# Optimization experiments

Measured on AMD Instinct MI355X. Metric: run time of the kernel, lower is better.

## Reference

```python
import jax, jax.numpy as jnp
import numpy as np
from jax import lax

B, C, H, W = 16, 256, 96, 96
G, K, RED = 4, 3, 4


def setup_inputs() -> dict:
    key = jax.random.key(0)
    ks = jax.random.split(key, 8)
    return {
        "x": jax.random.normal(ks[0], (B, C, H, W), jnp.float32),
        "w_k": jax.random.normal(ks[1], (G, C, K, K), jnp.float32) * 0.02,
        "b_k": jax.random.normal(ks[2], (G, C), jnp.float32) * 0.02,
        "w1": jax.random.normal(ks[3], (C // RED, C), jnp.float32) * 0.05,
        "b1": jax.random.normal(ks[4], (C // RED,), jnp.float32) * 0.02,
        "bn_g": jnp.ones((C // RED,), jnp.float32),
        "bn_b": jnp.zeros((C // RED,), jnp.float32),
        "bn_m": jnp.zeros((C // RED,), jnp.float32),
        "bn_v": jnp.ones((C // RED,), jnp.float32),
        "w2": jax.random.normal(ks[5], (C * G, C // RED), jnp.float32) * 0.05,
        "b2": jax.random.normal(ks[6], (C * G,), jnp.float32) * 0.02,
    }


def reference(x, w_k, b_k, w1, b1, bn_g, bn_b, bn_m, bn_v, w2, b2):
    eps = 1e-5

    def proj(t):  # t: (B, C, h, w) -> (B, C*G, h, w)
        h = jnp.einsum('oc,bchw->bohw', w1, t) + b1[None, :, None, None]
        h = (h - bn_m[None, :, None, None]) * (bn_g / jnp.sqrt(bn_v + eps))[None, :, None, None] + bn_b[None, :, None, None]
        h = jax.nn.gelu(h, approximate=False)
        return jnp.einsum('oc,bchw->bohw', w2, h) + b2[None, :, None, None]

    # AdaptiveAvgPool2d((K, K)) with H, W divisible by K -> uniform block mean
    pooled = x.reshape(B, C, K, H // K, K, W // K).mean(axis=(3, 5))  # (B, C, K, K)
    scale = proj(pooled).reshape(B, G, C, K, K)
    scale = jax.nn.softmax(scale, axis=1)
    weight = jnp.einsum('bgckl,gckl->bckl', scale, w_k)  # (B, C, K, K) dynamic depthwise kernels

    # dynamic bias from global average pooling
    s2 = proj(x.mean(axis=(2, 3), keepdims=True)).reshape(B, G, C)
    s2 = jax.nn.softmax(s2, axis=1)
    bias = jnp.einsum('bgc,gc->bc', s2, b_k)  # (B, C)

    pad = K // 2

    def conv_one(xb, wb):  # xb (C,H,W), wb (C,K,K): depthwise conv, SAME padding
        return lax.conv_general_dilated(
            xb[None], wb[:, None], window_strides=(1, 1),
            padding=[(pad, pad), (pad, pad)], feature_group_count=C)[0]

    out = jax.vmap(conv_one)(x, weight) + bias[:, :, None, None]
    return out
```

## Files before the change

kernel.cpp:

```cpp
#include <hip/hip_runtime.h>
#include <math.h>

#define BB 16
#define CC 256
#define HH 96
#define WW 96
#define TS 104

typedef float floatx4 __attribute__((ext_vector_type(4)));

__global__ __launch_bounds__(256) void pool_kernel(const float* __restrict__ x,
                                                   float* __restrict__ pooled) {
    const int bc = blockIdx.x;
    const float4* p4 = (const float4*)(x + (size_t)bc * (HH * WW));
    const int tid  = threadIdx.x;
    const int lane = tid & 63;
    const int wv   = tid >> 6;
    const int r_in = tid >> 3;
    const int c4   = tid & 7;
    __shared__ float red[9][4];

    float s[9];
    #pragma unroll
    for (int bi = 0; bi < 3; ++bi)
        #pragma unroll
        for (int bj = 0; bj < 3; ++bj) {
            float4 v = p4[(bi * 32 + r_in) * 24 + bj * 8 + c4];
            s[bi * 3 + bj] = v.x + v.y + v.z + v.w;
        }

    #pragma unroll
    for (int k = 0; k < 9; ++k) {
        float t = s[k];
        #pragma unroll
        for (int off = 32; off; off >>= 1) t += __shfl_down(t, off, 64);
        if (lane == 0) red[k][wv] = t;
    }
    __syncthreads();
    if (tid < 9)
        pooled[bc * 9 + tid] =
            (red[tid][0] + red[tid][1] + red[tid][2] + red[tid][3]) * (1.0f / 1024.0f);
}

__global__ __launch_bounds__(256) void proj_kernel(
    const float* __restrict__ pooled,
    const float* __restrict__ w1, const float* __restrict__ b1,
    const float* __restrict__ bn_g, const float* __restrict__ bn_b,
    const float* __restrict__ bn_m, const float* __restrict__ bn_v,
    const float* __restrict__ w2, const float* __restrict__ b2,
    const float* __restrict__ w_k, const float* __restrict__ b_k,
    float* __restrict__ weight, float* __restrict__ bias) {
    const int b = blockIdx.x / 10;
    const int p = blockIdx.x % 10;
    const int tid = threadIdx.x;

    __shared__ __align__(16) float t[CC];
    __shared__ __align__(16) float hbuf[64];
    __shared__ float hpart[256];

    if (p < 9) {
        t[tid] = pooled[(b * CC + tid) * 9 + p];
    } else {
        float s = 0.f;
        #pragma unroll
        for (int q = 0; q < 9; ++q) s += pooled[(b * CC + tid) * 9 + q];
        t[tid] = s * (1.0f / 9.0f);
    }
    __syncthreads();

    const int o = tid & 63, part = tid >> 6;
    {
        const float4* w1r = (const float4*)(w1 + o * CC + part * 64);
        const float4* tp  = (const float4*)(t + part * 64);
        float acc = 0.f;
        #pragma unroll
        for (int k = 0; k < 16; ++k) {
            float4 a = w1r[k], v = tp[k];
            acc += a.x * v.x + a.y * v.y + a.z * v.z + a.w * v.w;
        }
        hpart[tid] = acc;
    }
    __syncthreads();
    if (tid < 64) {
        float hsum = hpart[tid] + hpart[tid + 64] + hpart[tid + 128] +
                     hpart[tid + 192] + b1[tid];
        float hn = (hsum - bn_m[tid]) * (bn_g[tid] * rsqrtf(bn_v[tid] + 1e-5f)) + bn_b[tid];
        hbuf[tid] = 0.5f * hn * (1.0f + erff(hn * 0.70710678118654752f));
    }
    __syncthreads();

    float vals[4];
    #pragma unroll
    for (int q = 0; q < 4; ++q) {
        const int j = q * 256 + tid;
        const float4* w2r = (const float4*)(w2 + j * 64);
        const float4* hb  = (const float4*)hbuf;
        float a = b2[j];
        #pragma unroll
        for (int k = 0; k < 16; ++k) {
            float4 wv = w2r[k], hv = hb[k];
            a += wv.x * hv.x + wv.y * hv.y + wv.z * hv.z + wv.w * hv.w;
        }
        vals[q] = a;
    }
    float m = fmaxf(fmaxf(vals[0], vals[1]), fmaxf(vals[2], vals[3]));
    float e[4], sum = 0.f;
    #pragma unroll
    for (int q = 0; q < 4; ++q) { e[q] = expf(vals[q] - m); sum += e[q]; }
    const float rinv = 1.0f / sum;

    if (p < 9) {
        float ws = 0.f;
        #pragma unroll
        for (int q = 0; q < 4; ++q)
            ws += (e[q] * rinv) * w_k[(q * CC + tid) * 9 + p];
        weight[(b * CC + tid) * 9 + p] = ws;
    } else {
        float bs = 0.f;
        #pragma unroll
        for (int q = 0; q < 4; ++q)
            bs += (e[q] * rinv) * b_k[q * CC + tid];
        bias[b * CC + tid] = bs;
    }
}

__global__ __launch_bounds__(256) void dwconv_kernel(
    const float* __restrict__ x, const float* __restrict__ weight,
    const float* __restrict__ bias, float* __restrict__ out) {
    const int bc   = blockIdx.x >> 1;
    const int half = blockIdx.x & 1;
    const int r0   = half * 48;
    const float* plane = x + (size_t)bc * (HH * WW);
    float* oplane = out + (size_t)bc * (HH * WW);
    __shared__ __align__(16) float tile[50 * TS];
    const int tid = threadIdx.x;

    if (tid < 50) {
        tile[tid * TS + 3]   = 0.f;
        tile[tid * TS + 100] = 0.f;
    }
    if (tid < 98)
        tile[(half ? 49 * TS : 0) + 3 + tid] = 0.f;

    float wgt[9];
    #pragma unroll
    for (int k = 0; k < 9; ++k) wgt[k] = weight[bc * 9 + k];
    const float bs = bias[bc];

    {
        const int gstart = half ? 47 : 0;
        const int trow0  = half ? 0 : 1;
        const float4* p4 = (const float4*)plane + gstart * 24;
        float4* t4 = (float4*)tile + trow0 * (TS / 4);
        #pragma unroll
        for (int i = 0; i < 5; ++i) {
            const int idx4 = tid + 256 * i;
            if (idx4 < 1176) {
                const int r  = idx4 / 24;
                const int c4 = idx4 - r * 24;
                t4[r * (TS / 4) + 1 + c4] = p4[r * 24 + c4];
            }
        }
    }
    __syncthreads();

    #pragma unroll
    for (int j = 0; j < 2; ++j) {
        const int pidx = tid + 256 * j;
        if (pidx < 288) {
            const int pr = pidx / 24;
            const int pc = pidx - pr * 24;
            const int h0 = pr * 4;
            const int cb = 4 + pc * 4;

            float4 m[6]; float L[6], R[6];
            #pragma unroll
            for (int r = 0; r < 6; ++r) {
                const int a = (h0 + r) * TS + cb;
                m[r] = *(const float4*)(tile + a);
                L[r] = tile[a - 1];
                R[r] = tile[a + 4];
            }
            #pragma unroll
            for (int orow = 0; orow < 4; ++orow) {
                floatx4 acc = {bs, bs, bs, bs};
                #pragma unroll
                for (int r = 0; r < 3; ++r) {
                    const int rr = orow + r;
                    const float wl = wgt[r * 3 + 0], wc = wgt[r * 3 + 1],
                                wr = wgt[r * 3 + 2];
                    acc.x += wl * L[rr]   + wc * m[rr].x + wr * m[rr].y;
                    acc.y += wl * m[rr].x + wc * m[rr].y + wr * m[rr].z;
                    acc.z += wl * m[rr].y + wc * m[rr].z + wr * m[rr].w;
                    acc.w += wl * m[rr].z + wc * m[rr].w + wr * R[rr];
                }
                __builtin_nontemporal_store(
                    acc, (floatx4*)(oplane + (r0 + h0 + orow) * 96 + (cb - 4)));
            }
        }
    }
}

extern "C" void kernel_launch(void* const* d_in, const int* in_sizes, int n_in,
                              void* d_out, int out_size, void* d_ws, size_t ws_size,
                              hipStream_t stream) {
    const float* x    = (const float*)d_in[0];
    const float* w_k  = (const float*)d_in[1];
    const float* b_k  = (const float*)d_in[2];
    const float* w1   = (const float*)d_in[3];
    const float* b1   = (const float*)d_in[4];
    const float* bn_g = (const float*)d_in[5];
    const float* bn_b = (const float*)d_in[6];
    const float* bn_m = (const float*)d_in[7];
    const float* bn_v = (const float*)d_in[8];
    const float* w2   = (const float*)d_in[9];
    const float* b2   = (const float*)d_in[10];
    float* out = (float*)d_out;

    float* pooled = (float*)d_ws;
    float* weight = pooled + BB * CC * 9;
    float* bias   = weight + BB * CC * 9;

    pool_kernel<<<BB * CC, 256, 0, stream>>>(x, pooled);
    proj_kernel<<<BB * 10, 256, 0, stream>>>(pooled, w1, b1, bn_g, bn_b, bn_m,
                                             bn_v, w2, b2, w_k, b_k, weight, bias);
    dwconv_kernel<<<BB * CC * 2, 256, 0, stream>>>(x, weight, bias, out);
}
```

Baseline: 315.3 us.

## Fuse pool, projection and depthwise conv into one cooperative persistent kernel

Replaces the three separate launches with a single cooperative kernel that runs the pooling, projection/softmax and depthwise conv stages in grid-stride loops separated by grid-wide syncs. The aim is to remove inter-kernel launch gaps and tail effects. In exchange, the grid is limited to resident blocks, most blocks idle during the small projection stage, and the combined shared memory footprint may reduce occupancy. The three-kernel path is kept as a fallback if the cooperative launch fails.

```diff
diff --git a/kernel.cpp b/kernel.cpp
--- a/kernel.cpp
+++ b/kernel.cpp
@@ -1,5 +1,8 @@
 #include <hip/hip_runtime.h>
+#include <hip/hip_cooperative_groups.h>
 #include <math.h>
+
+namespace cg = cooperative_groups;
 
 #define BB 16
 #define CC 256
@@ -8,6 +11,205 @@
 #define TS 104
 
 typedef float floatx4 __attribute__((ext_vector_type(4)));
+
+__global__ __launch_bounds__(256) void fused_kernel(
+    const float* __restrict__ x,
+    const float* __restrict__ w_k, const float* __restrict__ b_k,
+    const float* __restrict__ w1, const float* __restrict__ b1,
+    const float* __restrict__ bn_g, const float* __restrict__ bn_b,
+    const float* __restrict__ bn_m, const float* __restrict__ bn_v,
+    const float* __restrict__ w2, const float* __restrict__ b2,
+    float* __restrict__ pooled, float* __restrict__ weight,
+    float* __restrict__ bias, float* __restrict__ out) {
+
+    __shared__ __align__(16) float tile[50 * TS];
+    __shared__ __align__(16) float t[CC];
+    __shared__ __align__(16) float hbuf[64];
+    __shared__ float hpart[256];
+    __shared__ float red[9][4];
+
+    const int tid  = threadIdx.x;
+    const int lane = tid & 63;
+    const int wv   = tid >> 6;
+    cg::grid_group grid = cg::this_grid();
+
+    {
+        const int r_in = tid >> 3;
+        const int c4   = tid & 7;
+        for (int bc = blockIdx.x; bc < BB * CC; bc += gridDim.x) {
+            const float4* p4 = (const float4*)(x + (size_t)bc * (HH * WW));
+            float s[9];
+            #pragma unroll
+            for (int bi = 0; bi < 3; ++bi)
+                #pragma unroll
+                for (int bj = 0; bj < 3; ++bj) {
+                    float4 v = p4[(bi * 32 + r_in) * 24 + bj * 8 + c4];
+                    s[bi * 3 + bj] = v.x + v.y + v.z + v.w;
+                }
+            #pragma unroll
+            for (int k = 0; k < 9; ++k) {
+                float tv = s[k];
+                #pragma unroll
+                for (int off = 32; off; off >>= 1) tv += __shfl_down(tv, off, 64);
+                if (lane == 0) red[k][wv] = tv;
+            }
+            __syncthreads();
+            if (tid < 9)
+                pooled[bc * 9 + tid] =
+                    (red[tid][0] + red[tid][1] + red[tid][2] + red[tid][3]) * (1.0f / 1024.0f);
+            __syncthreads();
+        }
+    }
+    __threadfence();
+    grid.sync();
+
+    for (int u = blockIdx.x; u < BB * 10; u += gridDim.x) {
+        const int b = u / 10;
+        const int p = u % 10;
+
+        if (p < 9) {
+            t[tid] = pooled[(b * CC + tid) * 9 + p];
+        } else {
+            float s = 0.f;
+            #pragma unroll
+            for (int q = 0; q < 9; ++q) s += pooled[(b * CC + tid) * 9 + q];
+            t[tid] = s * (1.0f / 9.0f);
+        }
+        __syncthreads();
+
+        const int o = tid & 63, part = tid >> 6;
+        {
+            const float4* w1r = (const float4*)(w1 + o * CC + part * 64);
+            const float4* tp  = (const float4*)(t + part * 64);
+            float acc = 0.f;
+            #pragma unroll
+            for (int k = 0; k < 16; ++k) {
+                float4 a = w1r[k], v = tp[k];
+                acc += a.x * v.x + a.y * v.y + a.z * v.z + a.w * v.w;
+            }
+            hpart[tid] = acc;
+        }
+        __syncthreads();
+        if (tid < 64) {
+            float hsum = hpart[tid] + hpart[tid + 64] + hpart[tid + 128] +
+                         hpart[tid + 192] + b1[tid];
+            float hn = (hsum - bn_m[tid]) * (bn_g[tid] * rsqrtf(bn_v[tid] + 1e-5f)) + bn_b[tid];
+            hbuf[tid] = 0.5f * hn * (1.0f + erff(hn * 0.70710678118654752f));
+        }
+        __syncthreads();
+
+        float vals[4];
+        #pragma unroll
+        for (int q = 0; q < 4; ++q) {
+            const int j = q * 256 + tid;
+            const float4* w2r = (const float4*)(w2 + j * 64);
+            const float4* hb  = (const float4*)hbuf;
+            float a = b2[j];
+            #pragma unroll
+            for (int k = 0; k < 16; ++k) {
+                float4 wvv = w2r[k], hv = hb[k];
+                a += wvv.x * hv.x + wvv.y * hv.y + wvv.z * hv.z + wvv.w * hv.w;
+            }
+            vals[q] = a;
+        }
+        float m = fmaxf(fmaxf(vals[0], vals[1]), fmaxf(vals[2], vals[3]));
+        float e[4], sum = 0.f;
+        #pragma unroll
+        for (int q = 0; q < 4; ++q) { e[q] = expf(vals[q] - m); sum += e[q]; }
+        const float rinv = 1.0f / sum;
+
+        if (p < 9) {
+            float ws = 0.f;
+            #pragma unroll
+            for (int q = 0; q < 4; ++q)
+                ws += (e[q] * rinv) * w_k[(q * CC + tid) * 9 + p];
+            weight[(b * CC + tid) * 9 + p] = ws;
+        } else {
+            float bs = 0.f;
+            #pragma unroll
+            for (int q = 0; q < 4; ++q)
+                bs += (e[q] * rinv) * b_k[q * CC + tid];
+            bias[b * CC + tid] = bs;
+        }
+        __syncthreads();
+    }
+    __threadfence();
+    grid.sync();
+
+    for (int hp = blockIdx.x; hp < BB * CC * 2; hp += gridDim.x) {
+        __syncthreads();
+        const int bc   = hp >> 1;
+        const int half = hp & 1;
+        const int r0   = half * 48;
+        const float* plane = x + (size_t)bc * (HH * WW);
+        float* oplane = out + (size_t)bc * (HH * WW);
+
+        if (tid < 50) {
+            tile[tid * TS + 3]   = 0.f;
+            tile[tid * TS + 100] = 0.f;
+        }
+        if (tid < 98)
+            tile[(half ? 49 * TS : 0) + 3 + tid] = 0.f;
+
+        float wgt[9];
+        #pragma unroll
+        for (int k = 0; k < 9; ++k) wgt[k] = weight[bc * 9 + k];
+        const float bs = bias[bc];
+
+        {
+            const int gstart = half ? 47 : 0;
+            const int trow0  = half ? 0 : 1;
+            const float4* p4 = (const float4*)plane + gstart * 24;
+            float4* t4 = (float4*)tile + trow0 * (TS / 4);
+            #pragma unroll
+            for (int i = 0; i < 5; ++i) {
+                const int idx4 = tid + 256 * i;
+                if (idx4 < 1176) {
+                    const int r  = idx4 / 24;
+                    const int c4 = idx4 - r * 24;
+                    t4[r * (TS / 4) + 1 + c4] = p4[r * 24 + c4];
+                }
+            }
+        }
+        __syncthreads();
+
+        #pragma unroll
+        for (int j = 0; j < 2; ++j) {
+            const int pidx = tid + 256 * j;
+            if (pidx < 288) {
+                const int pr = pidx / 24;
+                const int pc = pidx - pr * 24;
+                const int h0 = pr * 4;
+                const int cb = 4 + pc * 4;
+
+                float4 m[6]; float L[6], R[6];
+                #pragma unroll
+                for (int r = 0; r < 6; ++r) {
+                    const int a = (h0 + r) * TS + cb;
+                    m[r] = *(const float4*)(tile + a);
+                    L[r] = tile[a - 1];
+                    R[r] = tile[a + 4];
+                }
+                #pragma unroll
+                for (int orow = 0; orow < 4; ++orow) {
+                    floatx4 acc = {bs, bs, bs, bs};
+                    #pragma unroll
+                    for (int r = 0; r < 3; ++r) {
+                        const int rr = orow + r;
+                        const float wl = wgt[r * 3 + 0], wc = wgt[r * 3 + 1],
+                                    wr = wgt[r * 3 + 2];
+                        acc.x += wl * L[rr]   + wc * m[rr].x + wr * m[rr].y;
+                        acc.y += wl * m[rr].x + wc * m[rr].y + wr * m[rr].z;
+                        acc.z += wl * m[rr].y + wc * m[rr].z + wr * m[rr].w;
+                        acc.w += wl * m[rr].z + wc * m[rr].w + wr * R[rr];
+                    }
+                    __builtin_nontemporal_store(
+                        acc, (floatx4*)(oplane + (r0 + h0 + orow) * 96 + (cb - 4)));
+                }
+            }
+        }
+    }
+}
 
 __global__ __launch_bounds__(256) void pool_kernel(const float* __restrict__ x,
                                                    float* __restrict__ pooled) {
@@ -28,13 +230,12 @@
             float4 v = p4[(bi * 32 + r_in) * 24 + bj * 8 + c4];
             s[bi * 3 + bj] = v.x + v.y + v.z + v.w;
         }
-
     #pragma unroll
     for (int k = 0; k < 9; ++k) {
-        float t = s[k];
-        #pragma unroll
-        for (int off = 32; off; off >>= 1) t += __shfl_down(t, off, 64);
-        if (lane == 0) red[k][wv] = t;
+        float tv = s[k];
+        #pragma unroll
+        for (int off = 32; off; off >>= 1) tv += __shfl_down(tv, off, 64);
+        if (lane == 0) red[k][wv] = tv;
     }
     __syncthreads();
     if (tid < 9)
@@ -67,7 +268,6 @@
         t[tid] = s * (1.0f / 9.0f);
     }
     __syncthreads();
-
     const int o = tid & 63, part = tid >> 6;
     {
         const float4* w1r = (const float4*)(w1 + o * CC + part * 64);
@@ -88,7 +288,6 @@
         hbuf[tid] = 0.5f * hn * (1.0f + erff(hn * 0.70710678118654752f));
     }
     __syncthreads();
-
     float vals[4];
     #pragma unroll
     for (int q = 0; q < 4; ++q) {
@@ -98,8 +297,8 @@
         float a = b2[j];
         #pragma unroll
         for (int k = 0; k < 16; ++k) {
-            float4 wv = w2r[k], hv = hb[k];
-            a += wv.x * hv.x + wv.y * hv.y + wv.z * hv.z + wv.w * hv.w;
+            float4 wvv = w2r[k], hv = hb[k];
+            a += wvv.x * hv.x + wvv.y * hv.y + wvv.z * hv.z + wvv.w * hv.w;
         }
         vals[q] = a;
     }
@@ -108,7 +307,6 @@
     #pragma unroll
     for (int q = 0; q < 4; ++q) { e[q] = expf(vals[q] - m); sum += e[q]; }
     const float rinv = 1.0f / sum;
-
     if (p < 9) {
         float ws = 0.f;
         #pragma unroll
@@ -172,7 +370,6 @@
             const int pc = pidx - pr * 24;
             const int h0 = pr * 4;
             const int cb = 4 + pc * 4;
-
             float4 m[6]; float L[6], R[6];
             #pragma unroll
             for (int r = 0; r < 6; ++r) {
@@ -221,8 +418,32 @@
     float* weight = pooled + BB * CC * 9;
     float* bias   = weight + BB * CC * 9;
 
-    pool_kernel<<<BB * CC, 256, 0, stream>>>(x, pooled);
-    proj_kernel<<<BB * 10, 256, 0, stream>>>(pooled, w1, b1, bn_g, bn_b, bn_m,
-                                             bn_v, w2, b2, w_k, b_k, weight, bias);
-    dwconv_kernel<<<BB * CC * 2, 256, 0, stream>>>(x, weight, bias, out);
+    static int gridSize = 0;
+    if (gridSize == 0) {
+        int dev = 0;
+        (void)hipGetDevice(&dev);
+        int cus = 256;
+        (void)hipDeviceGetAttribute(&cus, hipDeviceAttributeMultiprocessorCount, dev);
+        int occ = 0;
+        (void)hipOccupancyMaxActiveBlocksPerMultiprocessor(&occ, fused_kernel, 256, 0);
+        if (occ < 1) occ = 1;
+        long g = (long)cus * occ;
+        if (g > BB * CC * 2) g = BB * CC * 2;
+        if (g < 1) g = 1;
+        gridSize = (int)g;
+    }
+
+    void* args[] = {(void*)&x,    (void*)&w_k,  (void*)&b_k,  (void*)&w1,
+                    (void*)&b1,   (void*)&bn_g, (void*)&bn_b, (void*)&bn_m,
+                    (void*)&bn_v, (void*)&w2,   (void*)&b2,   (void*)&pooled,
+                    (void*)&weight, (void*)&bias, (void*)&out};
+
+    hipError_t err = hipLaunchCooperativeKernel(fused_kernel, dim3(gridSize),
+                                                dim3(256), args, 0, stream);
+    if (err != hipSuccess) {
+        pool_kernel<<<BB * CC, 256, 0, stream>>>(x, pooled);
+        proj_kernel<<<BB * 10, 256, 0, stream>>>(pooled, w1, b1, bn_g, bn_b, bn_m,
+                                                 bn_v, w2, b2, w_k, b_k, weight, bias);
+        dwconv_kernel<<<BB * CC * 2, 256, 0, stream>>>(x, weight, bias, out);
+    }
 }
```

Result: slower. 459.0 us (+45.6%).

## Drop LDS tiling in depthwise conv; read halos directly from global

Applied to the files above, without the earlier changes.

The depthwise conv kernel no longer stages a half-plane tile in shared memory. One 576-thread block now covers a whole 96x96 plane, and each thread loads its 6 rows of float4 plus the left and right halo scalars straight from global memory, with boundary checks standing in for zero padding. This removes the LDS writes, the barrier and the duplicated halo rows between the two halves. In exchange, overlapping halo reads go to global memory and rely on the cache, and unaligned scalar loads are added.

```diff
diff --git a/kernel.cpp b/kernel.cpp
--- a/kernel.cpp
+++ b/kernel.cpp
@@ -5,7 +5,6 @@
 #define CC 256
 #define HH 96
 #define WW 96
-#define TS 104
 
 typedef float floatx4 __attribute__((ext_vector_type(4)));
 
@@ -124,80 +123,54 @@
     }
 }
 
-__global__ __launch_bounds__(256) void dwconv_kernel(
+__global__ __launch_bounds__(576) void dwconv_kernel(
     const float* __restrict__ x, const float* __restrict__ weight,
     const float* __restrict__ bias, float* __restrict__ out) {
-    const int bc   = blockIdx.x >> 1;
-    const int half = blockIdx.x & 1;
-    const int r0   = half * 48;
+    const int bc = blockIdx.x;
     const float* plane = x + (size_t)bc * (HH * WW);
     float* oplane = out + (size_t)bc * (HH * WW);
-    __shared__ __align__(16) float tile[50 * TS];
     const int tid = threadIdx.x;
-
-    if (tid < 50) {
-        tile[tid * TS + 3]   = 0.f;
-        tile[tid * TS + 100] = 0.f;
-    }
-    if (tid < 98)
-        tile[(half ? 49 * TS : 0) + 3 + tid] = 0.f;
+    const int pr  = tid / 24;
+    const int pc  = tid - pr * 24;
+    const int h0  = pr * 4;
+    const int c0  = pc * 4;
 
     float wgt[9];
     #pragma unroll
     for (int k = 0; k < 9; ++k) wgt[k] = weight[bc * 9 + k];
     const float bs = bias[bc];
 
-    {
-        const int gstart = half ? 47 : 0;
-        const int trow0  = half ? 0 : 1;
-        const float4* p4 = (const float4*)plane + gstart * 24;
-        float4* t4 = (float4*)tile + trow0 * (TS / 4);
-        #pragma unroll
-        for (int i = 0; i < 5; ++i) {
-            const int idx4 = tid + 256 * i;
-            if (idx4 < 1176) {
-                const int r  = idx4 / 24;
-                const int c4 = idx4 - r * 24;
-                t4[r * (TS / 4) + 1 + c4] = p4[r * 24 + c4];
-            }
-        }
-    }
-    __syncthreads();
-
-    #pragma unroll
-    for (int j = 0; j < 2; ++j) {
-        const int pidx = tid + 256 * j;
-        if (pidx < 288) {
-            const int pr = pidx / 24;
-            const int pc = pidx - pr * 24;
-            const int h0 = pr * 4;
-            const int cb = 4 + pc * 4;
-
-            float4 m[6]; float L[6], R[6];
-            #pragma unroll
-            for (int r = 0; r < 6; ++r) {
-                const int a = (h0 + r) * TS + cb;
-                m[r] = *(const float4*)(tile + a);
-                L[r] = tile[a - 1];
-                R[r] = tile[a + 4];
-            }
-            #pragma unroll
-            for (int orow = 0; orow < 4; ++orow) {
-                floatx4 acc = {bs, bs, bs, bs};
-                #pragma unroll
-                for (int r = 0; r < 3; ++r) {
-                    const int rr = orow + r;
-                    const float wl = wgt[r * 3 + 0], wc = wgt[r * 3 + 1],
-                                wr = wgt[r * 3 + 2];
-                    acc.x += wl * L[rr]   + wc * m[rr].x + wr * m[rr].y;
-                    acc.y += wl * m[rr].x + wc * m[rr].y + wr * m[rr].z;
-                    acc.z += wl * m[rr].y + wc * m[rr].z + wr * m[rr].w;
-                    acc.w += wl * m[rr].z + wc * m[rr].w + wr * R[rr];
-                }
-                __builtin_nontemporal_store(
-                    acc, (floatx4*)(oplane + (r0 + h0 + orow) * 96 + (cb - 4)));
-            }
-        }
+    float4 m[6]; float L[6], R[6];
+    #pragma unroll
+    for (int r = 0; r < 6; ++r) {
+        const int gr = h0 + r - 1;
+        if (gr >= 0 && gr < HH) {
+            const float* row = plane + gr * WW + c0;
+            m[r] = *(const float4*)row;
+            L[r] = (pc > 0)  ? row[-1] : 0.f;
+            R[r] = (pc < 23) ? row[4]  : 0.f;
+        } else {
+            m[r] = make_float4(0.f, 0.f, 0.f, 0.f);
+            L[r] = 0.f;
+            R[r] = 0.f;
+        }
+    }
+
+    #pragma unroll
+    for (int orow = 0; orow < 4; ++orow) {
+        floatx4 acc = {bs, bs, bs, bs};
+        #pragma unroll
+        for (int r = 0; r < 3; ++r) {
+            const int rr = orow + r;
+            const float wl = wgt[r * 3 + 0], wc = wgt[r * 3 + 1],
+                        wr = wgt[r * 3 + 2];
+            acc.x += wl * L[rr]   + wc * m[rr].x + wr * m[rr].y;
+            acc.y += wl * m[rr].x + wc * m[rr].y + wr * m[rr].z;
+            acc.z += wl * m[rr].y + wc * m[rr].z + wr * m[rr].w;
+            acc.w += wl * m[rr].z + wc * m[rr].w + wr * R[rr];
+        }
+        __builtin_nontemporal_store(
+            acc, (floatx4*)(oplane + (h0 + orow) * WW + c0));
     }
 }
 
@@ -224,5 +197,5 @@
     pool_kernel<<<BB * CC, 256, 0, stream>>>(x, pooled);
     proj_kernel<<<BB * 10, 256, 0, stream>>>(pooled, w1, b1, bn_g, bn_b, bn_m,
                                              bn_v, w2, b2, w_k, b_k, weight, bias);
-    dwconv_kernel<<<BB * CC * 2, 256, 0, stream>>>(x, weight, bias, out);
-}
+    dwconv_kernel<<<BB * CC, 576, 0, stream>>>(x, weight, bias, out);
+}
```

Result: no change. 312.2 us (-1.0%).
